# Optimization experiments

Measured on AMD Instinct MI355X. Metric: run time of the kernel, lower is better.

Reference implementation:

```python
import jax, jax.numpy as jnp
import numpy as np

N_STEPS = 3  # fixed propagation depth standing in for the BFS-guided delta_st recursion


def setup_inputs() -> dict:
    key = jax.random.key(0)
    ks = jax.random.split(key, 12)
    n, d, E = 32, 96, 256
    f32 = jnp.float32
    rn = lambda k, s, sc: jax.random.normal(k, s, f32) * sc
    return {
        "node_embeddings": rn(ks[0], (n, d), 1.0),
        "edges": jax.random.randint(ks[1], (E, 2), 0, n, jnp.int32),
        "w1": rn(ks[2], (4, 4, 3), 0.3), "b1": jnp.full((4,), 0.01, f32),
        "w2": rn(ks[3], (4, 4, 3), 0.3), "b2": jnp.full((4,), 0.01, f32),
        "w3": rn(ks[4], (4, 4, 3), 0.3), "b3": jnp.full((4,), 0.01, f32),
        "fc1_w": rn(ks[5], (16, 128), 0.2), "fc1_b": jnp.full((128,), 0.01, f32),
        "fc2_w": rn(ks[6], (128, 256), 0.1), "fc2_b": jnp.full((256,), 0.01, f32),
        "fc3_w": rn(ks[7], (256, 128), 0.1), "fc3_b": jnp.full((128,), 0.01, f32),
        "fc4_w": rn(ks[8], (128, 1), 0.1), "fc4_b": jnp.full((1,), 0.01, f32),
    }


def _conv1d(x, w, b, stride):
    # x: [B, C, L], w: [O, I, K]
    y = jax.lax.conv_general_dilated(x, w, (stride,), 'VALID',
                                     dimension_numbers=('NCH', 'OIH', 'NCH'))
    return y + b[None, :, None]


def _maxpool2(x):
    return jax.lax.reduce_window(x, -jnp.inf, jax.lax.max, (1, 1, 2), (1, 1, 2), 'VALID')


def _conv_pool_stack(x, w1, b1, w2, b2, w3, b3,
                     fc1_w, fc1_b, fc2_w, fc2_b, fc3_w, fc3_b, fc4_w, fc4_b):
    # x: [B, 4, 96] -> [B]
    h = _maxpool2(jax.nn.relu(_conv1d(x, w1, b1, 2)))   # [B,4,23]
    h = _maxpool2(jax.nn.relu(_conv1d(h, w2, b2, 1)))   # [B,4,10]
    h = _maxpool2(jax.nn.relu(_conv1d(h, w3, b3, 1)))   # [B,4,4]
    h = h.reshape(h.shape[0], -1)                       # [B,16]
    h = jax.nn.relu(h @ fc1_w + fc1_b)
    h = jax.nn.relu(h @ fc2_w + fc2_b)
    h = jax.nn.relu(h @ fc3_w + fc3_b)
    return (h @ fc4_w + fc4_b)[:, 0]


def reference(node_embeddings, edges, w1, b1, w2, b2, w3, b3,
              fc1_w, fc1_b, fc2_w, fc2_b, fc3_w, fc3_b, fc4_w, fc4_b):
    n, d = node_embeddings.shape
    E = edges.shape[0]
    u_idx, v_idx = edges[:, 0], edges[:, 1]

    # All (s, t) node pairs, flattened: P = n*n (s == t masked out below).
    s_idx, t_idx = jnp.meshgrid(jnp.arange(n), jnp.arange(n), indexing='ij')
    s_idx, t_idx = s_idx.reshape(-1), t_idx.reshape(-1)
    P = n * n

    se = node_embeddings[s_idx]  # [P, d]
    te = node_embeddings[t_idx]  # [P, d]
    ue = node_embeddings[u_idx]  # [E, d]
    ve = node_embeddings[v_idx]  # [E, d]

    # stuv input: [P, E, 4, d] -> [P*E, 4, d]
    stuv = jnp.stack([
        jnp.broadcast_to(se[:, None, :], (P, E, d)),
        jnp.broadcast_to(te[:, None, :], (P, E, d)),
        jnp.broadcast_to(ue[None, :, :], (P, E, d)),
        jnp.broadcast_to(ve[None, :, :], (P, E, d)),
    ], axis=2).reshape(P * E, 4, d)

    preds = _conv_pool_stack(stuv, w1, b1, w2, b2, w3, b3,
                             fc1_w, fc1_b, fc2_w, fc2_b,
                             fc3_w, fc3_b, fc4_w, fc4_b).reshape(P, E)

    # zero out s == t pairs (the original skips them)
    preds = preds * (s_idx != t_idx).astype(preds.dtype)[:, None]

    # delta_st: propagate unit mass from s through the per-pair sparse routing
    # matrix R[u, v] = preds[p, e] for N_STEPS hops, accumulating arrivals.
    x = jax.nn.one_hot(s_idx, n, dtype=preds.dtype)  # [P, n]
    rbc = jnp.zeros((n,), preds.dtype)
    for _ in range(N_STEPS):
        gathered = x[:, u_idx] * preds                      # [P, E]
        x = jnp.zeros((P, n), preds.dtype).at[:, v_idx].add(gathered)
        rbc = rbc + x.sum(axis=0)

    return rbc / jnp.sum(rbc)
```

## Files before the change

kernel.cpp:

```cpp
#include <hip/hip_runtime.h>

constexpr int F_ELEMS = 4 * 32 * 4 * 48;
constexpr int PREDS_OFF = F_ELEMS;
constexpr int RBCP_OFF = PREDS_OFF + 1024 * 256;
constexpr int CNT_OFF = RBCP_OFF + 2048;
constexpr int W1P_OFF = CNT_OFF + 16;
constexpr int W2P_OFF = W1P_OFF + 2048;
constexpr int W3P_OFF = W2P_OFF + 16384;

typedef __attribute__((ext_vector_type(8))) short short8;
typedef __attribute__((ext_vector_type(4))) short short4v;
typedef __attribute__((ext_vector_type(4))) float f32x4;

__device__ __forceinline__ unsigned short f2bf(float x) {
    unsigned u = __float_as_uint(x);
    u += 0x7FFF + ((u >> 16) & 1);
    return (unsigned short)(u >> 16);
}

template <int CTRL>
__device__ __forceinline__ float qp(float x) {
    return __int_as_float(__builtin_amdgcn_update_dpp(
        0, __float_as_int(x), CTRL, 0xF, 0xF, true));
}

__global__ void prep_all(const float* __restrict__ emb, const float* __restrict__ w1,
                         const float* __restrict__ fc1_w, const float* __restrict__ fc2_w,
                         const float* __restrict__ fc3_w,
                         float* __restrict__ F, unsigned short* __restrict__ W1p,
                         unsigned short* __restrict__ W2p, unsigned short* __restrict__ W3p,
                         float* __restrict__ rbcp_zero) {
    int b = blockIdx.x;
    if (b < 96) {
        int idx = b * 256 + threadIdx.x;
        int i = idx % 48;
        int o = (idx / 48) % 4;
        int node = (idx / 192) % 32;
        int c = idx / 6144;
        float acc = 0.f;
        if (i < 46) {
#pragma unroll
            for (int k = 0; k < 3; k++) acc += w1[(o * 4 + c) * 3 + k] * emb[node * 96 + 2 * i + k];
        }
        F[idx] = acc;
        return;
    }
    if (b < 112) {
        int t = (b - 96) * 256 + threadIdx.x;
        int j = t & 7, lane = (t >> 3) & 63, mt = t >> 9;
        int k = (lane >> 4) * 8 + j, n = mt * 16 + (lane & 15);
        float w = (k < 16) ? fc1_w[k * 128 + n] : 0.f;
        W1p[t] = f2bf(w);
        return;
    }
    if (b < 240) {
        int t = (b - 112) * 256 + threadIdx.x;
        int j = t & 7, lane = (t >> 3) & 63, ks = (t >> 9) & 3, mt = t >> 11;
        int k = ks * 32 + (lane >> 4) * 8 + j, n = mt * 16 + (lane & 15);
        W2p[t] = f2bf(fc2_w[k * 256 + n]);
        return;
    }
    if (b < 368) {
        int t = (b - 240) * 256 + threadIdx.x;
        int j = t & 7, lane = (t >> 3) & 63, ks = (t >> 9) & 7, mt = t >> 12;
        int k = ks * 32 + (lane >> 4) * 8 + j, n = mt * 16 + (lane & 15);
        W3p[t] = f2bf(fc3_w[k * 128 + n]);
        return;
    }
    for (int k = threadIdx.x; k < 2064; k += 256) rbcp_zero[k] = 0.f;
}

__global__ __launch_bounds__(256, 4)
void mlp_kernel(const float* __restrict__ F, const int* __restrict__ edges,
                const float* __restrict__ b1v,
                const float* __restrict__ w2, const float* __restrict__ b2,
                const float* __restrict__ w3, const float* __restrict__ b3,
                const float* __restrict__ fc1_b, const float* __restrict__ fc2_b,
                const float* __restrict__ fc3_b,
                const float* __restrict__ fc4_w, const float* __restrict__ fc4_b,
                const unsigned short* __restrict__ W1p, const unsigned short* __restrict__ W2p,
                const unsigned short* __restrict__ W3p,
                float* __restrict__ preds) {
    __shared__ __align__(16) float smem[8448];
    unsigned short* X1 = (unsigned short*)smem;
    unsigned short* X3h = (unsigned short*)smem;
    unsigned short* X2 = (unsigned short*)(smem + 4096);
    float* part = smem + 8192;

    const int tid = threadIdx.x;
    const int p = blockIdx.x >> 2;
    const int e0 = (blockIdx.x & 3) * 64;
    const int s = p >> 5, t = p & 31;
    if (s == t) return;

    const int gsample = tid >> 2, o = tid & 3;
    float h1[23];
    {
        const int e = e0 + gsample;
        const int u = edges[2 * e], v = edges[2 * e + 1];
        const f32x4* F0 = (const f32x4*)(F + ((0 * 32 + s) * 4 + o) * 48);
        const f32x4* F1 = (const f32x4*)(F + ((1 * 32 + t) * 4 + o) * 48);
        const f32x4* F2 = (const f32x4*)(F + ((2 * 32 + u) * 4 + o) * 48);
        const f32x4* F3 = (const f32x4*)(F + ((3 * 32 + v) * 4 + o) * 48);
        const float bb = b1v[o];
        float pre[46];
#pragma unroll
        for (int q = 0; q < 12; q++) {
            f32x4 x = F0[q] + F1[q] + F2[q] + F3[q];
#pragma unroll
            for (int z = 0; z < 4; z++) {
                int i = 4 * q + z;
                if (i < 46) pre[i] = fmaxf(x[z] + bb, 0.f);
            }
        }
#pragma unroll
        for (int j = 0; j < 23; j++) h1[j] = fmaxf(pre[2 * j], pre[2 * j + 1]);
    }
    float h2[10];
    {
        float wm[4][3];
#pragma unroll
        for (int m = 0; m < 4; m++)
#pragma unroll
            for (int k = 0; k < 3; k++) wm[m][k] = w2[o * 12 + (o ^ m) * 3 + k];
        const float bb = b2[o];
        float win[4][3];
#pragma unroll
        for (int j = 0; j < 2; j++) {
            float x = h1[j];
            win[0][j] = x;
            win[1][j] = qp<0xB1>(x);
            win[2][j] = qp<0x4E>(x);
            win[3][j] = qp<0x1B>(x);
        }
        float pre[20];
#pragma unroll
        for (int i = 0; i < 20; i++) {
            float x = h1[i + 2];
            win[0][(i + 2) % 3] = x;
            win[1][(i + 2) % 3] = qp<0xB1>(x);
            win[2][(i + 2) % 3] = qp<0x4E>(x);
            win[3][(i + 2) % 3] = qp<0x1B>(x);
            float acc = bb;
#pragma unroll
            for (int m = 0; m < 4; m++)
#pragma unroll
                for (int k = 0; k < 3; k++)
                    acc = fmaf(wm[m][k], win[m][(i + k) % 3], acc);
            pre[i] = fmaxf(acc, 0.f);
        }
#pragma unroll
        for (int j = 0; j < 10; j++) h2[j] = fmaxf(pre[2 * j], pre[2 * j + 1]);
    }
    {
        float wm[4][3];
#pragma unroll
        for (int m = 0; m < 4; m++)
#pragma unroll
            for (int k = 0; k < 3; k++) wm[m][k] = w3[o * 12 + (o ^ m) * 3 + k];
        const float bb = b3[o];
        float win[4][3];
#pragma unroll
        for (int j = 0; j < 2; j++) {
            float x = h2[j];
            win[0][j] = x;
            win[1][j] = qp<0xB1>(x);
            win[2][j] = qp<0x4E>(x);
            win[3][j] = qp<0x1B>(x);
        }
        float pre[8];
#pragma unroll
        for (int i = 0; i < 8; i++) {
            float x = h2[i + 2];
            win[0][(i + 2) % 3] = x;
            win[1][(i + 2) % 3] = qp<0xB1>(x);
            win[2][(i + 2) % 3] = qp<0x4E>(x);
            win[3][(i + 2) % 3] = qp<0x1B>(x);
            float acc = bb;
#pragma unroll
            for (int m = 0; m < 4; m++)
#pragma unroll
                for (int k = 0; k < 3; k++)
                    acc = fmaf(wm[m][k], win[m][(i + k) % 3], acc);
            pre[i] = fmaxf(acc, 0.f);
        }
        short4v pk;
#pragma unroll
        for (int l = 0; l < 4; l++)
            pk[l] = (short)f2bf(fmaxf(pre[2 * l], pre[2 * l + 1]));
        *(short4v*)(X1 + (((o >> 1) * 64 + gsample) * 8) + (o & 1) * 4) = pk;
        short4v z4 = (short4v){0, 0, 0, 0};
        *(short4v*)(X1 + ((((o >> 1) + 2) * 64 + gsample) * 8) + (o & 1) * 4) = z4;
    }
    __syncthreads();
    const int lane = tid & 63, wave = tid >> 6;
    const int mrow = lane & 15, quad = lane >> 4;
    {
        const short8* W1v = (const short8*)W1p;
        short8 bnt[4];
#pragma unroll
        for (int nt = 0; nt < 4; nt++)
            bnt[nt] = *(const short8*)(X1 + (quad * 64 + nt * 16 + mrow) * 8);
        f32x4 acc1[2][4];
#pragma unroll
        for (int a = 0; a < 2; a++)
#pragma unroll
            for (int b = 0; b < 4; b++) acc1[a][b] = (f32x4){0.f, 0.f, 0.f, 0.f};
#pragma unroll
        for (int mtl = 0; mtl < 2; mtl++) {
            const int mt = wave * 2 + mtl;
            short8 ah = W1v[mt * 64 + lane];
#pragma unroll
            for (int nt = 0; nt < 4; nt++)
                acc1[mtl][nt] = __builtin_amdgcn_mfma_f32_16x16x32_bf16(ah, bnt[nt], acc1[mtl][nt], 0, 0, 0);
        }
#pragma unroll
        for (int mtl = 0; mtl < 2; mtl++) {
            const int mt = wave * 2 + mtl;
            const int n0 = mt * 16 + quad * 4;
            f32x4 b4 = *(const f32x4*)(fc1_b + n0);
#pragma unroll
            for (int nt = 0; nt < 4; nt++) {
                short4v pk;
#pragma unroll
                for (int r = 0; r < 4; r++)
                    pk[r] = (short)f2bf(fmaxf(acc1[mtl][nt][r] + b4[r], 0.f));
                *(short4v*)(X2 + ((n0 >> 3) * 64 + nt * 16 + mrow) * 8 + (n0 & 7)) = pk;
            }
        }
    }
    __syncthreads();
    const short8* W2v = (const short8*)W2p;
    const short8* W3v = (const short8*)W3p;
    f32x4 acc3[2][4];
#pragma unroll
    for (int a = 0; a < 2; a++)
#pragma unroll
        for (int b = 0; b < 4; b++) acc3[a][b] = (f32x4){0.f, 0.f, 0.f, 0.f};
#pragma unroll
    for (int h = 0; h < 2; h++) {
        f32x4 acc2[2][4];
#pragma unroll
        for (int a = 0; a < 2; a++)
#pragma unroll
            for (int b = 0; b < 4; b++) acc2[a][b] = (f32x4){0.f, 0.f, 0.f, 0.f};
#pragma unroll
        for (int ks = 0; ks < 4; ks++) {
            short8 bfr[4];
#pragma unroll
            for (int nt = 0; nt < 4; nt++)
                bfr[nt] = *(const short8*)(X2 + ((ks * 4 + quad) * 64 + nt * 16 + mrow) * 8);
#pragma unroll
            for (int mtl = 0; mtl < 2; mtl++) {
                const int mt = h * 8 + wave * 2 + mtl;
                short8 ah = W2v[(mt * 4 + ks) * 64 + lane];
#pragma unroll
                for (int nt = 0; nt < 4; nt++)
                    acc2[mtl][nt] = __builtin_amdgcn_mfma_f32_16x16x32_bf16(ah, bfr[nt], acc2[mtl][nt], 0, 0, 0);
            }
        }
#pragma unroll
        for (int mtl = 0; mtl < 2; mtl++) {
            const int mt = h * 8 + wave * 2 + mtl;
            const int n0 = mt * 16 + quad * 4;
            const int kl = n0 - h * 128;
            f32x4 b4 = *(const f32x4*)(fc2_b + n0);
#pragma unroll
            for (int nt = 0; nt < 4; nt++) {
                short4v pk;
#pragma unroll
                for (int r = 0; r < 4; r++)
                    pk[r] = (short)f2bf(fmaxf(acc2[mtl][nt][r] + b4[r], 0.f));
                *(short4v*)(X3h + ((kl >> 3) * 64 + nt * 16 + mrow) * 8 + (kl & 7)) = pk;
            }
        }
        __syncthreads();
#pragma unroll
        for (int ksl = 0; ksl < 4; ksl++) {
            const int ks = h * 4 + ksl;
            short8 bfr[4];
#pragma unroll
            for (int nt = 0; nt < 4; nt++)
                bfr[nt] = *(const short8*)(X3h + ((ksl * 4 + quad) * 64 + nt * 16 + mrow) * 8);
#pragma unroll
            for (int mtl = 0; mtl < 2; mtl++) {
                const int mt = wave * 2 + mtl;
                short8 ah = W3v[(mt * 8 + ks) * 64 + lane];
#pragma unroll
                for (int nt = 0; nt < 4; nt++)
                    acc3[mtl][nt] = __builtin_amdgcn_mfma_f32_16x16x32_bf16(ah, bfr[nt], acc3[mtl][nt], 0, 0, 0);
            }
        }
        __syncthreads();
    }
    {
        float p4[4] = {0.f, 0.f, 0.f, 0.f};
#pragma unroll
        for (int mtl = 0; mtl < 2; mtl++) {
            const int mt = wave * 2 + mtl;
            const int n0 = mt * 16 + quad * 4;
            f32x4 b4 = *(const f32x4*)(fc3_b + n0);
            f32x4 w44 = *(const f32x4*)(fc4_w + n0);
#pragma unroll
            for (int nt = 0; nt < 4; nt++)
#pragma unroll
                for (int r = 0; r < 4; r++)
                    p4[nt] = fmaf(fmaxf(acc3[mtl][nt][r] + b4[r], 0.f), w44[r], p4[nt]);
        }
#pragma unroll
        for (int nt = 0; nt < 4; nt++) {
            p4[nt] += __shfl_xor(p4[nt], 16, 64);
            p4[nt] += __shfl_xor(p4[nt], 32, 64);
        }
        if (quad == 0) {
#pragma unroll
            for (int nt = 0; nt < 4; nt++)
                part[wave * 64 + nt * 16 + mrow] = p4[nt];
        }
    }
    __syncthreads();
    if (tid < 64) {
        float pred = part[tid] + part[64 + tid] + part[128 + tid] + part[192 + tid] + fc4_b[0];
        preds[p * 256 + e0 + tid] = pred;
    }
}

__global__ __launch_bounds__(256)
void prop_norm(const int* __restrict__ edges, const float* __restrict__ preds,
               float* __restrict__ rbc_part, int* __restrict__ counter,
               float* __restrict__ out) {
    const int tid = threadIdx.x;
    const int wave = tid >> 6, lane = tid & 63;
    const int p = blockIdx.x * 4 + wave;
    const int s = p >> 5, t = p & 31;
    __shared__ float xw[4][32], xnw[4][32], raccw[4][32];
    __shared__ float red[8][32];
    __shared__ int lastflag;
    int u[4], v[4];
    float pr[4];
#pragma unroll
    for (int j = 0; j < 4; j++) {
        int e = lane + 64 * j;
        u[j] = edges[2 * e];
        v[j] = edges[2 * e + 1];
        pr[j] = preds[p * 256 + e];
    }
    if (lane < 32) { xw[wave][lane] = (lane == s) ? 1.f : 0.f; raccw[wave][lane] = 0.f; }
    const bool active = (s != t);
    for (int step = 0; step < 3; step++) {
        if (lane < 32) xnw[wave][lane] = 0.f;
        __syncthreads();
        if (active) {
#pragma unroll
            for (int j = 0; j < 4; j++)
                atomicAdd(&xnw[wave][v[j]], xw[wave][u[j]] * pr[j]);
        }
        __syncthreads();
        if (lane < 32) { raccw[wave][lane] += xnw[wave][lane]; xw[wave][lane] = xnw[wave][lane]; }
        __syncthreads();
    }
    if (active && lane < 32) atomicAdd(&rbc_part[(p & 63) * 32 + lane], raccw[wave][lane]);
    __syncthreads();
    if (tid == 0) lastflag = (atomicAdd(counter, 1) == 255);
    __syncthreads();
    if (!lastflag) return;
    const int node = tid & 31, sub = tid >> 5;
    float vv = 0.f;
#pragma unroll
    for (int g = 0; g < 8; g++)
        vv += atomicAdd(&rbc_part[(sub * 8 + g) * 32 + node], 0.f);
    red[sub][node] = vv;
    __syncthreads();
    if (tid < 32) {
        float acc = 0.f;
#pragma unroll
        for (int sb = 0; sb < 8; sb++) acc += red[sb][tid];
        float tot = acc;
#pragma unroll
        for (int mask = 1; mask < 32; mask <<= 1) tot += __shfl_xor(tot, mask, 32);
        out[tid] = acc / tot;
    }
}

extern "C" void kernel_launch(void* const* d_in, const int* in_sizes, int n_in,
                              void* d_out, int out_size, void* d_ws, size_t ws_size,
                              hipStream_t stream) {
    const float* emb = (const float*)d_in[0];
    const int* edges = (const int*)d_in[1];
    const float* w1 = (const float*)d_in[2];
    const float* b1 = (const float*)d_in[3];
    const float* w2 = (const float*)d_in[4];
    const float* b2 = (const float*)d_in[5];
    const float* w3 = (const float*)d_in[6];
    const float* b3 = (const float*)d_in[7];
    const float* fc1_w = (const float*)d_in[8];
    const float* fc1_b = (const float*)d_in[9];
    const float* fc2_w = (const float*)d_in[10];
    const float* fc2_b = (const float*)d_in[11];
    const float* fc3_w = (const float*)d_in[12];
    const float* fc3_b = (const float*)d_in[13];
    const float* fc4_w = (const float*)d_in[14];
    const float* fc4_b = (const float*)d_in[15];

    float* ws = (float*)d_ws;
    float* F = ws;
    float* preds = ws + PREDS_OFF;
    float* rbc_part = ws + RBCP_OFF;
    int* counter = (int*)(ws + CNT_OFF);
    unsigned short* W1p = (unsigned short*)(ws + W1P_OFF);
    unsigned short* W2p = (unsigned short*)(ws + W2P_OFF);
    unsigned short* W3p = (unsigned short*)(ws + W3P_OFF);
    float* out = (float*)d_out;

    prep_all<<<dim3(369), dim3(256), 0, stream>>>(emb, w1, fc1_w, fc2_w, fc3_w,
                                                  F, W1p, W2p, W3p, rbc_part);
    mlp_kernel<<<dim3(4096), dim3(256), 0, stream>>>(
        F, edges, b1, w2, b2, w3, b3, fc1_b, fc2_b, fc3_b,
        fc4_w, fc4_b, W1p, W2p, W3p, preds);
    prop_norm<<<dim3(256), dim3(256), 0, stream>>>(edges, preds, rbc_part, counter, out);
}
```

Before: 167.7 us.

## Split fc2/fc3 chain into quarter chunks to shrink shared memory and accumulators

Restructures the fused fc2→fc3 loop from two halves to four quarters, with each wave computing one fc2 M-tile per quarter instead of two. This halves the acc2 register footprint and shrinks the X3 staging buffer, so shared memory drops from 8448 to 6144 floats and X2/part are relocated. The aim is higher occupancy through lower register and LDS use, at the cost of twice as many __syncthreads barriers and shorter MFMA bursts between them.

```diff
diff --git a/kernel.cpp b/kernel.cpp
--- a/kernel.cpp
+++ b/kernel.cpp
@@ -81,11 +81,11 @@
                 const unsigned short* __restrict__ W1p, const unsigned short* __restrict__ W2p,
                 const unsigned short* __restrict__ W3p,
                 float* __restrict__ preds) {
-    __shared__ __align__(16) float smem[8448];
+    __shared__ __align__(16) float smem[6144];
     unsigned short* X1 = (unsigned short*)smem;
-    unsigned short* X3h = (unsigned short*)smem;
-    unsigned short* X2 = (unsigned short*)(smem + 4096);
-    float* part = smem + 8192;
+    unsigned short* X3q = (unsigned short*)smem;
+    unsigned short* X2 = (unsigned short*)(smem + 2048);
+    float* part = smem + 2048;
 
     const int tid = threadIdx.x;
     const int p = blockIdx.x >> 2;
@@ -238,50 +238,43 @@
 #pragma unroll
         for (int b = 0; b < 4; b++) acc3[a][b] = (f32x4){0.f, 0.f, 0.f, 0.f};
 #pragma unroll
-    for (int h = 0; h < 2; h++) {
-        f32x4 acc2[2][4];
-#pragma unroll
-        for (int a = 0; a < 2; a++)
-#pragma unroll
-            for (int b = 0; b < 4; b++) acc2[a][b] = (f32x4){0.f, 0.f, 0.f, 0.f};
+    for (int q = 0; q < 4; q++) {
+        const int mt2 = q * 4 + wave;
+        f32x4 acc2[4];
+#pragma unroll
+        for (int b = 0; b < 4; b++) acc2[b] = (f32x4){0.f, 0.f, 0.f, 0.f};
 #pragma unroll
         for (int ks = 0; ks < 4; ks++) {
             short8 bfr[4];
 #pragma unroll
             for (int nt = 0; nt < 4; nt++)
                 bfr[nt] = *(const short8*)(X2 + ((ks * 4 + quad) * 64 + nt * 16 + mrow) * 8);
-#pragma unroll
-            for (int mtl = 0; mtl < 2; mtl++) {
-                const int mt = h * 8 + wave * 2 + mtl;
-                short8 ah = W2v[(mt * 4 + ks) * 64 + lane];
-#pragma unroll
-                for (int nt = 0; nt < 4; nt++)
-                    acc2[mtl][nt] = __builtin_amdgcn_mfma_f32_16x16x32_bf16(ah, bfr[nt], acc2[mtl][nt], 0, 0, 0);
-            }
-        }
-#pragma unroll
-        for (int mtl = 0; mtl < 2; mtl++) {
-            const int mt = h * 8 + wave * 2 + mtl;
-            const int n0 = mt * 16 + quad * 4;
-            const int kl = n0 - h * 128;
+            short8 ah = W2v[(mt2 * 4 + ks) * 64 + lane];
+#pragma unroll
+            for (int nt = 0; nt < 4; nt++)
+                acc2[nt] = __builtin_amdgcn_mfma_f32_16x16x32_bf16(ah, bfr[nt], acc2[nt], 0, 0, 0);
+        }
+        {
+            const int n0 = mt2 * 16 + quad * 4;
+            const int kl = n0 - q * 64;
             f32x4 b4 = *(const f32x4*)(fc2_b + n0);
 #pragma unroll
             for (int nt = 0; nt < 4; nt++) {
                 short4v pk;
 #pragma unroll
                 for (int r = 0; r < 4; r++)
-                    pk[r] = (short)f2bf(fmaxf(acc2[mtl][nt][r] + b4[r], 0.f));
-                *(short4v*)(X3h + ((kl >> 3) * 64 + nt * 16 + mrow) * 8 + (kl & 7)) = pk;
+                    pk[r] = (short)f2bf(fmaxf(acc2[nt][r] + b4[r], 0.f));
+                *(short4v*)(X3q + ((kl >> 3) * 64 + nt * 16 + mrow) * 8 + (kl & 7)) = pk;
             }
         }
         __syncthreads();
 #pragma unroll
-        for (int ksl = 0; ksl < 4; ksl++) {
-            const int ks = h * 4 + ksl;
+        for (int ksl = 0; ksl < 2; ksl++) {
+            const int ks = q * 2 + ksl;
             short8 bfr[4];
 #pragma unroll
             for (int nt = 0; nt < 4; nt++)
-                bfr[nt] = *(const short8*)(X3h + ((ksl * 4 + quad) * 64 + nt * 16 + mrow) * 8);
+                bfr[nt] = *(const short8*)(X3q + ((ksl * 4 + quad) * 64 + nt * 16 + mrow) * 8);
 #pragma unroll
             for (int mtl = 0; mtl < 2; mtl++) {
                 const int mt = wave * 2 + mtl;
```

New measurement: 176.0 us. 1.05x slower.
